# Performance work log

Measured on AMD Instinct MI355X. Metric: run time of the kernel, lower is better.

Reference implementation:

```python
import jax, jax.numpy as jnp
import numpy as np
from jax.scipy.special import logsumexp

_INF = 1e8
_GAMMA_MIN = 1e-4


def _cosine_cost(x, y):
    # 1 - cosine similarity, batched: [B,M,D] x [B,N,D] -> [B,M,N]
    xn = x / jnp.clip(jnp.linalg.norm(x, axis=-1, keepdims=True), 1e-8)
    yn = y / jnp.clip(jnp.linalg.norm(y, axis=-1, keepdims=True), 1e-8)
    return 1.0 - jnp.einsum('bmd,bnd->bmn', xn, yn)


def _soft_dtw_alignment(cost, gv):
    B, M, N = cost.shape
    dt = cost.dtype
    ii = jnp.arange(M)          # full diagonal index range, masked per step

    # ---- forward DP: R[b, i+1, j+1] = C[i,j] + softmin(R[i,j], R[i,j+1], R[i+1,j]) ----
    R0 = jnp.full((B, M + 1, N + 1), _INF, dtype=dt).at[:, 0, 0].set(0.0)

    def fstep(R, d):
        jj = d - ii
        valid = (jj >= 0) & (jj < N)            # (M,)
        jjc = jnp.clip(jj, 0, N - 1)
        ip, jp = ii + 1, jjc + 1
        p = jnp.stack([R[:, ip - 1, jp - 1],
                       R[:, ip - 1, jp],
                       R[:, ip, jp - 1]], axis=-1)          # (B, M, 3)
        soft = -gv * logsumexp(p / -gv, axis=-1)            # soft-min
        new = cost[:, ii, jjc] + soft                       # (B, M)
        cur = R[:, ip, jp]
        R = R.at[:, ip, jp].set(jnp.where(valid[None, :], new, cur))
        return R, None

    R, _ = jax.lax.scan(fstep, R0, jnp.arange(M + N - 1))
    distance = R[:, M, N]

    # ---- backward DP for alignment matrix E ----
    E0 = jnp.zeros((B, M + 2, N + 2), dtype=dt).at[:, M, N].set(1.0)
    Re = jnp.full((B, M + 2, N + 2), -_INF, dtype=dt).at[:, :M + 1, :N + 1].set(R)
    Ce = jnp.zeros((B, M + 2, N + 2), dtype=dt).at[:, 1:M + 1, 1:N + 1].set(cost)

    def bstep(E, d):
        jj = d - ii
        valid = (jj >= 0) & (jj < N)
        jjc = jnp.clip(jj, 0, N - 1)
        ip, jp = ii + 1, jjc + 1
        rc = Re[:, ip, jp]
        wd = jnp.exp(jnp.clip((Re[:, ip + 1, jp + 1] - Ce[:, ip + 1, jp + 1] - rc) / gv, -50, 50))
        wn = jnp.exp(jnp.clip((Re[:, ip + 1, jp] - Ce[:, ip + 1, jp] - rc) / gv, -50, 50))
        wr = jnp.exp(jnp.clip((Re[:, ip, jp + 1] - Ce[:, ip, jp + 1] - rc) / gv, -50, 50))
        new = E[:, ip + 1, jp + 1] * wd + E[:, ip + 1, jp] * wn + E[:, ip, jp + 1] * wr
        cur = E[:, ip, jp]
        E = E.at[:, ip, jp].set(jnp.where(valid[None, :], new, cur))
        return E, None

    E, _ = jax.lax.scan(bstep, E0, jnp.arange(M + N - 3, -1, -1))
    alignment = E[:, 1:M + 1, 1:N + 1]
    return alignment, distance


def setup_inputs() -> dict:
    key = jax.random.key(0)
    k1, k2 = jax.random.split(key)
    B, M, N, D = 8, 256, 256, 512
    x = jax.random.normal(k1, (B, M, D), dtype=jnp.float32)
    y = jax.random.normal(k2, (B, N, D), dtype=jnp.float32)
    gamma = jnp.asarray(1.0, dtype=jnp.float32)   # learned nn.Parameter
    return {"x": x, "y": y, "gamma": gamma}


def reference(x, y, gamma):
    cost = _cosine_cost(x, y)
    gv = jnp.maximum(jnp.abs(gamma), _GAMMA_MIN)   # effective gamma
    alignment, distance = _soft_dtw_alignment(cost, gv)
    return alignment, distance
```

## Files before the change

### kernel.cpp

```cpp
#include <hip/hip_runtime.h>

#define USTR 192

#define EXP2F(x) __builtin_amdgcn_exp2f(x)
#define LOG2F(x) __builtin_amdgcn_logf(x)

__device__ __forceinline__ void ld4(float d[4], const float* p) {
  float4 v = *(const float4*)p;
  d[0] = v.x; d[1] = v.y; d[2] = v.z; d[3] = v.w;
}

__device__ __forceinline__ float dpp_shr1_f(float x) {
  int r = __builtin_amdgcn_update_dpp(0, __float_as_int(x),
                                      0x138 , 0xF, 0xF, true);
  return __int_as_float(r);
}
__device__ __forceinline__ int dpp_shr1_i(int x) {
  return __builtin_amdgcn_update_dpp(0, x, 0x138, 0xF, 0xF, true);
}

__global__ void __launch_bounds__(256) cost_gemm(const float* __restrict__ x,
                                                 const float* __restrict__ y,
                                                 const float* __restrict__ gamma,
                                                 float* __restrict__ mAll) {
  int b = blockIdx.z, mt = blockIdx.y, nt = blockIdx.x;
  int m0 = mt * 32, n0 = nt * 64;
  __shared__ float Xs[2][32][36];
  __shared__ float Ys[2][32][68];
  __shared__ float RxS[32];
  __shared__ float RyS[64];
  int tid = threadIdx.x;
  int row = tid >> 2, cq = tid & 3;
  int tx = tid & 15, ty = tid >> 4;
  const float* xb = x + ((size_t)b * 256 + m0) * 512;
  const float* yb = y + ((size_t)b * 256 + n0) * 512;
  float acc[2][4] = {};
  float sx = 0.f, sy = 0.f;
  float4 xv0, xv1, yv0, yv1;

  auto loadTile = [&](int k0) {
    if (tid < 128) {
      xv0 = *(const float4*)(xb + (size_t)row * 512 + k0 + cq * 4);
      xv1 = *(const float4*)(xb + (size_t)row * 512 + k0 + 16 + cq * 4);
    }
    yv0 = *(const float4*)(yb + (size_t)row * 512 + k0 + cq * 4);
    yv1 = *(const float4*)(yb + (size_t)row * 512 + k0 + 16 + cq * 4);
  };
  auto stageTile = [&](int buf) {
    if (tid < 128) {
      sx += xv0.x*xv0.x + xv0.y*xv0.y + xv0.z*xv0.z + xv0.w*xv0.w
          + xv1.x*xv1.x + xv1.y*xv1.y + xv1.z*xv1.z + xv1.w*xv1.w;
      Xs[buf][cq*4+0][row] = xv0.x; Xs[buf][cq*4+1][row] = xv0.y;
      Xs[buf][cq*4+2][row] = xv0.z; Xs[buf][cq*4+3][row] = xv0.w;
      Xs[buf][16+cq*4+0][row] = xv1.x; Xs[buf][16+cq*4+1][row] = xv1.y;
      Xs[buf][16+cq*4+2][row] = xv1.z; Xs[buf][16+cq*4+3][row] = xv1.w;
    }
    sy += yv0.x*yv0.x + yv0.y*yv0.y + yv0.z*yv0.z + yv0.w*yv0.w
        + yv1.x*yv1.x + yv1.y*yv1.y + yv1.z*yv1.z + yv1.w*yv1.w;
    Ys[buf][cq*4+0][row] = yv0.x; Ys[buf][cq*4+1][row] = yv0.y;
    Ys[buf][cq*4+2][row] = yv0.z; Ys[buf][cq*4+3][row] = yv0.w;
    Ys[buf][16+cq*4+0][row] = yv1.x; Ys[buf][16+cq*4+1][row] = yv1.y;
    Ys[buf][16+cq*4+2][row] = yv1.z; Ys[buf][16+cq*4+3][row] = yv1.w;
  };

  loadTile(0);
  stageTile(0);
  for (int t = 0; t < 16; ++t) {
    __syncthreads();
    if (t < 15) loadTile((t + 1) * 32);
    int cb = t & 1;
#pragma unroll
    for (int kk = 0; kk < 32; ++kk) {
      float2 av = *(const float2*)(&Xs[cb][kk][ty * 2]);
      float4 bv = *(const float4*)(&Ys[cb][kk][tx * 4]);
      acc[0][0] += av.x * bv.x; acc[0][1] += av.x * bv.y;
      acc[0][2] += av.x * bv.z; acc[0][3] += av.x * bv.w;
      acc[1][0] += av.y * bv.x; acc[1][1] += av.y * bv.y;
      acc[1][2] += av.y * bv.z; acc[1][3] += av.y * bv.w;
    }
    if (t < 15) stageTile(cb ^ 1);
  }

  sy += __shfl_xor(sy, 1, 64); sy += __shfl_xor(sy, 2, 64);
  if (tid < 128) { sx += __shfl_xor(sx, 1, 64); sx += __shfl_xor(sx, 2, 64); }
  if (cq == 0) {
    RyS[row] = 1.0f / fmaxf(sqrtf(sy), 1e-8f);
    if (tid < 128) RxS[row] = 1.0f / fmaxf(sqrtf(sx), 1e-8f);
  }
  __syncthreads();

  float gv = fmaxf(fabsf(gamma[0]), 1e-4f);
  float ig2 = 1.4426950408889634f / gv;
  float rx[2], ry[4];
#pragma unroll
  for (int r = 0; r < 2; ++r) rx[r] = RxS[ty * 2 + r];
#pragma unroll
  for (int c = 0; c < 4; ++c) ry[c] = RyS[tx * 4 + c];
  int l = nt * 16 + tx;
  int v = mt * 16 + ty;
  int u = v + l;
  float4 stm[2];
#pragma unroll
  for (int r = 0; r < 2; ++r) {
    float c0 = (1.0f - acc[r][0] * rx[r] * ry[0]) * ig2;
    float c1 = (1.0f - acc[r][1] * rx[r] * ry[1]) * ig2;
    float c2 = (1.0f - acc[r][2] * rx[r] * ry[2]) * ig2;
    float c3 = (1.0f - acc[r][3] * rx[r] * ry[3]) * ig2;
    stm[r] = (float4){EXP2F(-c0), EXP2F(-c1), EXP2F(-c2), EXP2F(-c3)};
  }
  float* mpF = mAll + ((size_t)b * USTR + u) * 512 + l * 8;
  *(float4*)(mpF)     = stm[0];
  *(float4*)(mpF + 4) = stm[1];
}

template<int DIR>
__device__ __forceinline__ void run_chain(const float* __restrict__ mAll,
                                          float* __restrict__ pAll,
                                          float* __restrict__ QepAll,
                                          float gl, int blk, int l,
                                          float* __restrict__ dist_out) {
  int b = blk & 7;
  const float* mb = mAll + (size_t)b * USTR * 512 + (DIR ? (63 - l) * 8 : l * 8);
  float* pb = pAll + (size_t)blk * USTR * 512 + l * 8;
  float* qe = QepAll + ((size_t)blk * 64 + l) * 24;
  float Pp0 = 0.f, Pp1 = 0.f, Pp2 = 0.f, Pp3 = 0.f;
  float bot0 = 0.f, bot1 = 0.f;
  int Q = 0;
  float ucar = (l == 0) ? 1.0f : 0.f;
  float presh0 = 0.f, presh1 = 0.f;
  int adj = 0;
  float A0[8], A1[8], A2[8], A3[8], A4[8], A5[8], A6[8], A7[8];
  float A8[8], A9[8], A10[8], A11[8], A12[8], A13[8], A14[8], A15[8];
  auto loadC = [&](int t, float* buf) {
    int u = t > 190 ? 190 : t;
    int pu = DIR ? 190 - u : u;
    const float* p = mb + (size_t)pu * 512;
    float q0[4], q1[4];
    ld4(q0, p); ld4(q1, p + 4);
    if (DIR) {
      buf[0] = q1[3]; buf[1] = q1[2]; buf[2] = q1[1]; buf[3] = q1[0];
      buf[4] = q0[3]; buf[5] = q0[2]; buf[6] = q0[1]; buf[7] = q0[0];
    } else {
      buf[0] = q0[0]; buf[1] = q0[1]; buf[2] = q0[2]; buf[3] = q0[3];
      buf[4] = q1[0]; buf[5] = q1[1]; buf[6] = q1[2]; buf[7] = q1[3];
    }
  };
  auto body = [&](int t, const float* mm) {
    float s0 = ldexpf(presh0, adj);
    float s1 = ldexpf(presh1, adj);
    float v0 = mm[0] * (Pp0 + s0 + ucar);
    float v1 = mm[1] * (Pp1 + v0 + Pp0);
    float v2 = mm[2] * (Pp2 + v1 + Pp1);
    float v3 = mm[3] * (Pp3 + v2 + Pp2);
    float w0 = mm[4] * (v0 + s1 + s0);
    float w1 = mm[5] * (v1 + w0 + v0);
    float w2 = mm[6] * (v2 + w1 + v1);
    float w3 = mm[7] * (v3 + w2 + v2);
    float* sp = pb + (size_t)t * 512;
    *(float4*)(sp)     = (float4){v0, v1, v2, v3};
    *(float4*)(sp + 4) = (float4){w0, w1, w2, w3};
    Pp0 = w0; Pp1 = w1; Pp2 = w2; Pp3 = w3;
    ucar = s1; bot0 = v3; bot1 = w3;
    if (DIR == 0 && l == 63 && t == 190)
      dist_out[b] = (-(float)Q - LOG2F(w3)) * gl;
    presh0 = dpp_shr1_f(bot0);
    presh1 = dpp_shr1_f(bot1);
  };
  auto renorm = [&](int tEnd) {
    if ((unsigned)(tEnd - l) <= 127u) {
      int e = (int)((__float_as_uint(Pp3) >> 23) & 255u) - 127;
      Pp0 = ldexpf(Pp0, -e); Pp1 = ldexpf(Pp1, -e);
      Pp2 = ldexpf(Pp2, -e); Pp3 = ldexpf(Pp3, -e);
      ucar = ldexpf(ucar, -e);
      bot0 = ldexpf(bot0, -e); bot1 = ldexpf(bot1, -e);
      Q += e;
    }
    presh0 = dpp_shr1_f(bot0);
    presh1 = dpp_shr1_f(bot1);
    adj = dpp_shr1_i(Q) - Q;
  };
  loadC(0, A0);  loadC(1, A1);  loadC(2, A2);  loadC(3, A3);
  loadC(4, A4);  loadC(5, A5);  loadC(6, A6);  loadC(7, A7);
  loadC(8, A8);  loadC(9, A9);  loadC(10, A10); loadC(11, A11);
  loadC(12, A12); loadC(13, A13); loadC(14, A14); loadC(15, A15);
  for (int it = 0; it < 12; ++it) {
    int s = it * 16;
    qe[2 * it] = (float)Q;
    body(s + 0, A0); loadC(s + 16, A0);
    body(s + 1, A1); loadC(s + 17, A1);
    body(s + 2, A2); loadC(s + 18, A2);
    body(s + 3, A3); loadC(s + 19, A3);
    body(s + 4, A4); loadC(s + 20, A4);
    body(s + 5, A5); loadC(s + 21, A5);
    body(s + 6, A6); loadC(s + 22, A6);
    body(s + 7, A7); loadC(s + 23, A7);
    renorm(s + 7);
    qe[2 * it + 1] = (float)Q;
    body(s + 8,  A8);  loadC(s + 24, A8);
    body(s + 9,  A9);  loadC(s + 25, A9);
    body(s + 10, A10); loadC(s + 26, A10);
    body(s + 11, A11); loadC(s + 27, A11);
    body(s + 12, A12); loadC(s + 28, A12);
    body(s + 13, A13); loadC(s + 29, A13);
    body(s + 14, A14); loadC(s + 30, A14);
    body(s + 15, A15); loadC(s + 31, A15);
    renorm(s + 15);
  }
}

__global__ void __launch_bounds__(64, 1) pass_kernel(const float* __restrict__ mAll,
                                                     float* __restrict__ pAll,
                                                     float* __restrict__ QepAll,
                                                     const float* __restrict__ gamma,
                                                     float* __restrict__ dist_out) {
  int blk = blockIdx.x, l = threadIdx.x;
  float gv = fmaxf(fabsf(gamma[0]), 1e-4f);
  float gl = gv * 0.6931471805599453f;
  if (blk < 8) run_chain<0>(mAll, pAll, QepAll, gl, blk, l, dist_out);
  else         run_chain<1>(mAll, pAll, QepAll, gl, blk, l, dist_out);
}

__global__ void __launch_bounds__(256) e_kernel(const float* __restrict__ mAll,
                                                const float* __restrict__ pAll,
                                                const float* __restrict__ QepAll,
                                                float* __restrict__ out) {
  int tid = blockIdx.x * 256 + threadIdx.x;
  int l = tid & 63;
  int r = (tid >> 6) & 255;
  int b = tid >> 14;
  int v = r >> 1, rf = r & 1;
  int uF = v + l;
  int uR = 190 - v - l;
  const float* pF  = pAll + ((size_t)b * USTR + uF) * 512 + l * 8 + rf * 4;
  const float* pRv = pAll + ((size_t)(8 + b) * USTR + uR) * 512 + (63 - l) * 8 + (1 - rf) * 4;
  const float* mF  = mAll + ((size_t)b * USTR + uF) * 512 + l * 8 + rf * 4;
  float P[4], Bv[4], M[4];
  ld4(P, pF); ld4(Bv, pRv); ld4(M, mF);
  float Qf = QepAll[((size_t)b * 64 + l) * 24 + (uF >> 3)];
  float Qb = QepAll[((size_t)(8 + b) * 64 + (63 - l)) * 24 + (uR >> 3)];
  float Zp = pAll[((size_t)b * USTR + 190) * 512 + 511];
  float Zq = QepAll[((size_t)b * 64 + 63) * 24 + 23];
  int e = (int)(Qf + Qb - Zq);
  float inv = 1.0f / Zp;
  float4 o;
  o.x = ldexpf(P[0] * Bv[3] / M[0] * inv, e);
  o.y = ldexpf(P[1] * Bv[2] / M[1] * inv, e);
  o.z = ldexpf(P[2] * Bv[1] / M[2] * inv, e);
  o.w = ldexpf(P[3] * Bv[0] / M[3] * inv, e);
  *(float4*)(out + (size_t)b * 65536 + (size_t)r * 256 + 4 * l) = o;
}

extern "C" void kernel_launch(void* const* d_in, const int* in_sizes, int n_in,
                              void* d_out, int out_size, void* d_ws, size_t ws_size,
                              hipStream_t stream) {
  const float* x = (const float*)d_in[0];
  const float* y = (const float*)d_in[1];
  const float* gamma = (const float*)d_in[2];
  float* out = (float*)d_out;
  float* ws = (float*)d_ws;

  const size_t PMAT_M = (size_t)8 * USTR * 512;
  const size_t PMAT_P = (size_t)16 * USTR * 512;
  float* mAll   = ws + 4096;
  float* pAll   = mAll + PMAT_M;
  float* QepAll = pAll + PMAT_P;

  cost_gemm<<<dim3(4, 8, 8), 256, 0, stream>>>(x, y, gamma, mAll);
  pass_kernel<<<16, 64, 0, stream>>>(mAll, pAll, QepAll, gamma, out + 524288);
  e_kernel<<<512, 256, 0, stream>>>(mAll, pAll, QepAll, out);
}
```

Baseline: 108.0 us.

## Fuse GEMM, DP chain and E-pass into one persistent kernel with grid barriers

```diff
diff --git a/kernel.cpp b/kernel.cpp
--- a/kernel.cpp
+++ b/kernel.cpp
@@ -1,6 +1,7 @@
 #include <hip/hip_runtime.h>
 
 #define USTR 192
+#define NBLK 256
 
 #define EXP2F(x) __builtin_amdgcn_exp2f(x)
 #define LOG2F(x) __builtin_amdgcn_logf(x)
@@ -19,98 +20,23 @@
   return __builtin_amdgcn_update_dpp(0, x, 0x138, 0xF, 0xF, true);
 }
 
-__global__ void __launch_bounds__(256) cost_gemm(const float* __restrict__ x,
-                                                 const float* __restrict__ y,
-                                                 const float* __restrict__ gamma,
-                                                 float* __restrict__ mAll) {
-  int b = blockIdx.z, mt = blockIdx.y, nt = blockIdx.x;
-  int m0 = mt * 32, n0 = nt * 64;
-  __shared__ float Xs[2][32][36];
-  __shared__ float Ys[2][32][68];
-  __shared__ float RxS[32];
-  __shared__ float RyS[64];
-  int tid = threadIdx.x;
-  int row = tid >> 2, cq = tid & 3;
-  int tx = tid & 15, ty = tid >> 4;
-  const float* xb = x + ((size_t)b * 256 + m0) * 512;
-  const float* yb = y + ((size_t)b * 256 + n0) * 512;
-  float acc[2][4] = {};
-  float sx = 0.f, sy = 0.f;
-  float4 xv0, xv1, yv0, yv1;
-
-  auto loadTile = [&](int k0) {
-    if (tid < 128) {
-      xv0 = *(const float4*)(xb + (size_t)row * 512 + k0 + cq * 4);
-      xv1 = *(const float4*)(xb + (size_t)row * 512 + k0 + 16 + cq * 4);
-    }
-    yv0 = *(const float4*)(yb + (size_t)row * 512 + k0 + cq * 4);
-    yv1 = *(const float4*)(yb + (size_t)row * 512 + k0 + 16 + cq * 4);
-  };
-  auto stageTile = [&](int buf) {
-    if (tid < 128) {
-      sx += xv0.x*xv0.x + xv0.y*xv0.y + xv0.z*xv0.z + xv0.w*xv0.w
-          + xv1.x*xv1.x + xv1.y*xv1.y + xv1.z*xv1.z + xv1.w*xv1.w;
-      Xs[buf][cq*4+0][row] = xv0.x; Xs[buf][cq*4+1][row] = xv0.y;
-      Xs[buf][cq*4+2][row] = xv0.z; Xs[buf][cq*4+3][row] = xv0.w;
-      Xs[buf][16+cq*4+0][row] = xv1.x; Xs[buf][16+cq*4+1][row] = xv1.y;
-      Xs[buf][16+cq*4+2][row] = xv1.z; Xs[buf][16+cq*4+3][row] = xv1.w;
-    }
-    sy += yv0.x*yv0.x + yv0.y*yv0.y + yv0.z*yv0.z + yv0.w*yv0.w
-        + yv1.x*yv1.x + yv1.y*yv1.y + yv1.z*yv1.z + yv1.w*yv1.w;
-    Ys[buf][cq*4+0][row] = yv0.x; Ys[buf][cq*4+1][row] = yv0.y;
-    Ys[buf][cq*4+2][row] = yv0.z; Ys[buf][cq*4+3][row] = yv0.w;
-    Ys[buf][16+cq*4+0][row] = yv1.x; Ys[buf][16+cq*4+1][row] = yv1.y;
-    Ys[buf][16+cq*4+2][row] = yv1.z; Ys[buf][16+cq*4+3][row] = yv1.w;
-  };
-
-  loadTile(0);
-  stageTile(0);
-  for (int t = 0; t < 16; ++t) {
-    __syncthreads();
-    if (t < 15) loadTile((t + 1) * 32);
-    int cb = t & 1;
-#pragma unroll
-    for (int kk = 0; kk < 32; ++kk) {
-      float2 av = *(const float2*)(&Xs[cb][kk][ty * 2]);
-      float4 bv = *(const float4*)(&Ys[cb][kk][tx * 4]);
-      acc[0][0] += av.x * bv.x; acc[0][1] += av.x * bv.y;
-      acc[0][2] += av.x * bv.z; acc[0][3] += av.x * bv.w;
-      acc[1][0] += av.y * bv.x; acc[1][1] += av.y * bv.y;
-      acc[1][2] += av.y * bv.z; acc[1][3] += av.y * bv.w;
-    }
-    if (t < 15) stageTile(cb ^ 1);
-  }
-
-  sy += __shfl_xor(sy, 1, 64); sy += __shfl_xor(sy, 2, 64);
-  if (tid < 128) { sx += __shfl_xor(sx, 1, 64); sx += __shfl_xor(sx, 2, 64); }
-  if (cq == 0) {
-    RyS[row] = 1.0f / fmaxf(sqrtf(sy), 1e-8f);
-    if (tid < 128) RxS[row] = 1.0f / fmaxf(sqrtf(sx), 1e-8f);
-  }
+__device__ __forceinline__ void grid_barrier(unsigned* cnt, unsigned* flag) {
   __syncthreads();
-
-  float gv = fmaxf(fabsf(gamma[0]), 1e-4f);
-  float ig2 = 1.4426950408889634f / gv;
-  float rx[2], ry[4];
-#pragma unroll
-  for (int r = 0; r < 2; ++r) rx[r] = RxS[ty * 2 + r];
-#pragma unroll
-  for (int c = 0; c < 4; ++c) ry[c] = RyS[tx * 4 + c];
-  int l = nt * 16 + tx;
-  int v = mt * 16 + ty;
-  int u = v + l;
-  float4 stm[2];
-#pragma unroll
-  for (int r = 0; r < 2; ++r) {
-    float c0 = (1.0f - acc[r][0] * rx[r] * ry[0]) * ig2;
-    float c1 = (1.0f - acc[r][1] * rx[r] * ry[1]) * ig2;
-    float c2 = (1.0f - acc[r][2] * rx[r] * ry[2]) * ig2;
-    float c3 = (1.0f - acc[r][3] * rx[r] * ry[3]) * ig2;
-    stm[r] = (float4){EXP2F(-c0), EXP2F(-c1), EXP2F(-c2), EXP2F(-c3)};
-  }
-  float* mpF = mAll + ((size_t)b * USTR + u) * 512 + l * 8;
-  *(float4*)(mpF)     = stm[0];
-  *(float4*)(mpF + 4) = stm[1];
+  if (threadIdx.x == 0) {
+    unsigned old = __hip_atomic_fetch_add(cnt, 1u, __ATOMIC_ACQ_REL,
+                                          __HIP_MEMORY_SCOPE_AGENT);
+    if (old == NBLK - 1) {
+      __hip_atomic_store(flag, 1u, __ATOMIC_RELEASE, __HIP_MEMORY_SCOPE_AGENT);
+    } else {
+      int guard = 0;
+      while (!__hip_atomic_load(flag, __ATOMIC_ACQUIRE,
+                                __HIP_MEMORY_SCOPE_AGENT)) {
+        __builtin_amdgcn_s_sleep(8);
+        if (++guard > (1 << 22)) break;
+      }
+    }
+  }
+  __syncthreads();
 }
 
 template<int DIR>
@@ -208,46 +134,147 @@
   }
 }
 
-__global__ void __launch_bounds__(64, 1) pass_kernel(const float* __restrict__ mAll,
-                                                     float* __restrict__ pAll,
-                                                     float* __restrict__ QepAll,
-                                                     const float* __restrict__ gamma,
-                                                     float* __restrict__ dist_out) {
-  int blk = blockIdx.x, l = threadIdx.x;
-  float gv = fmaxf(fabsf(gamma[0]), 1e-4f);
-  float gl = gv * 0.6931471805599453f;
-  if (blk < 8) run_chain<0>(mAll, pAll, QepAll, gl, blk, l, dist_out);
-  else         run_chain<1>(mAll, pAll, QepAll, gl, blk, l, dist_out);
-}
-
-__global__ void __launch_bounds__(256) e_kernel(const float* __restrict__ mAll,
-                                                const float* __restrict__ pAll,
-                                                const float* __restrict__ QepAll,
-                                                float* __restrict__ out) {
-  int tid = blockIdx.x * 256 + threadIdx.x;
-  int l = tid & 63;
-  int r = (tid >> 6) & 255;
-  int b = tid >> 14;
-  int v = r >> 1, rf = r & 1;
-  int uF = v + l;
-  int uR = 190 - v - l;
-  const float* pF  = pAll + ((size_t)b * USTR + uF) * 512 + l * 8 + rf * 4;
-  const float* pRv = pAll + ((size_t)(8 + b) * USTR + uR) * 512 + (63 - l) * 8 + (1 - rf) * 4;
-  const float* mF  = mAll + ((size_t)b * USTR + uF) * 512 + l * 8 + rf * 4;
-  float P[4], Bv[4], M[4];
-  ld4(P, pF); ld4(Bv, pRv); ld4(M, mF);
-  float Qf = QepAll[((size_t)b * 64 + l) * 24 + (uF >> 3)];
-  float Qb = QepAll[((size_t)(8 + b) * 64 + (63 - l)) * 24 + (uR >> 3)];
-  float Zp = pAll[((size_t)b * USTR + 190) * 512 + 511];
-  float Zq = QepAll[((size_t)b * 64 + 63) * 24 + 23];
-  int e = (int)(Qf + Qb - Zq);
-  float inv = 1.0f / Zp;
-  float4 o;
-  o.x = ldexpf(P[0] * Bv[3] / M[0] * inv, e);
-  o.y = ldexpf(P[1] * Bv[2] / M[1] * inv, e);
-  o.z = ldexpf(P[2] * Bv[1] / M[2] * inv, e);
-  o.w = ldexpf(P[3] * Bv[0] / M[3] * inv, e);
-  *(float4*)(out + (size_t)b * 65536 + (size_t)r * 256 + 4 * l) = o;
+__global__ void __launch_bounds__(256, 1)
+fused_kernel(const float* __restrict__ x, const float* __restrict__ y,
+             const float* __restrict__ gamma, unsigned* __restrict__ bar,
+             float* __restrict__ mAll, float* __restrict__ pAll,
+             float* __restrict__ QepAll, float* __restrict__ out) {
+
+  {
+    int blk = blockIdx.x;
+    int nt = blk & 3, mt = (blk >> 2) & 7, b = blk >> 5;
+    int m0 = mt * 32, n0 = nt * 64;
+    __shared__ float Xs[2][32][36];
+    __shared__ float Ys[2][32][68];
+    __shared__ float RxS[32];
+    __shared__ float RyS[64];
+    int tid = threadIdx.x;
+    int row = tid >> 2, cq = tid & 3;
+    int tx = tid & 15, ty = tid >> 4;
+    const float* xb = x + ((size_t)b * 256 + m0) * 512;
+    const float* yb = y + ((size_t)b * 256 + n0) * 512;
+    float acc[2][4] = {};
+    float sx = 0.f, sy = 0.f;
+    float4 xv0, xv1, yv0, yv1;
+
+    auto loadTile = [&](int k0) {
+      if (tid < 128) {
+        xv0 = *(const float4*)(xb + (size_t)row * 512 + k0 + cq * 4);
+        xv1 = *(const float4*)(xb + (size_t)row * 512 + k0 + 16 + cq * 4);
+      }
+      yv0 = *(const float4*)(yb + (size_t)row * 512 + k0 + cq * 4);
+      yv1 = *(const float4*)(yb + (size_t)row * 512 + k0 + 16 + cq * 4);
+    };
+    auto stageTile = [&](int buf) {
+      if (tid < 128) {
+        sx += xv0.x*xv0.x + xv0.y*xv0.y + xv0.z*xv0.z + xv0.w*xv0.w
+            + xv1.x*xv1.x + xv1.y*xv1.y + xv1.z*xv1.z + xv1.w*xv1.w;
+        Xs[buf][cq*4+0][row] = xv0.x; Xs[buf][cq*4+1][row] = xv0.y;
+        Xs[buf][cq*4+2][row] = xv0.z; Xs[buf][cq*4+3][row] = xv0.w;
+        Xs[buf][16+cq*4+0][row] = xv1.x; Xs[buf][16+cq*4+1][row] = xv1.y;
+        Xs[buf][16+cq*4+2][row] = xv1.z; Xs[buf][16+cq*4+3][row] = xv1.w;
+      }
+      sy += yv0.x*yv0.x + yv0.y*yv0.y + yv0.z*yv0.z + yv0.w*yv0.w
+          + yv1.x*yv1.x + yv1.y*yv1.y + yv1.z*yv1.z + yv1.w*yv1.w;
+      Ys[buf][cq*4+0][row] = yv0.x; Ys[buf][cq*4+1][row] = yv0.y;
+      Ys[buf][cq*4+2][row] = yv0.z; Ys[buf][cq*4+3][row] = yv0.w;
+      Ys[buf][16+cq*4+0][row] = yv1.x; Ys[buf][16+cq*4+1][row] = yv1.y;
+      Ys[buf][16+cq*4+2][row] = yv1.z; Ys[buf][16+cq*4+3][row] = yv1.w;
+    };
+
+    loadTile(0);
+    stageTile(0);
+    for (int t = 0; t < 16; ++t) {
+      __syncthreads();
+      if (t < 15) loadTile((t + 1) * 32);
+      int cb = t & 1;
+#pragma unroll
+      for (int kk = 0; kk < 32; ++kk) {
+        float2 av = *(const float2*)(&Xs[cb][kk][ty * 2]);
+        float4 bv = *(const float4*)(&Ys[cb][kk][tx * 4]);
+        acc[0][0] += av.x * bv.x; acc[0][1] += av.x * bv.y;
+        acc[0][2] += av.x * bv.z; acc[0][3] += av.x * bv.w;
+        acc[1][0] += av.y * bv.x; acc[1][1] += av.y * bv.y;
+        acc[1][2] += av.y * bv.z; acc[1][3] += av.y * bv.w;
+      }
+      if (t < 15) stageTile(cb ^ 1);
+    }
+
+    sy += __shfl_xor(sy, 1, 64); sy += __shfl_xor(sy, 2, 64);
+    if (tid < 128) { sx += __shfl_xor(sx, 1, 64); sx += __shfl_xor(sx, 2, 64); }
+    if (cq == 0) {
+      RyS[row] = 1.0f / fmaxf(sqrtf(sy), 1e-8f);
+      if (tid < 128) RxS[row] = 1.0f / fmaxf(sqrtf(sx), 1e-8f);
+    }
+    __syncthreads();
+
+    float gv = fmaxf(fabsf(gamma[0]), 1e-4f);
+    float ig2 = 1.4426950408889634f / gv;
+    float rx[2], ry[4];
+#pragma unroll
+    for (int r = 0; r < 2; ++r) rx[r] = RxS[ty * 2 + r];
+#pragma unroll
+    for (int c = 0; c < 4; ++c) ry[c] = RyS[tx * 4 + c];
+    int l = nt * 16 + tx;
+    int v = mt * 16 + ty;
+    int u = v + l;
+    float4 stm[2];
+#pragma unroll
+    for (int r = 0; r < 2; ++r) {
+      float c0 = (1.0f - acc[r][0] * rx[r] * ry[0]) * ig2;
+      float c1 = (1.0f - acc[r][1] * rx[r] * ry[1]) * ig2;
+      float c2 = (1.0f - acc[r][2] * rx[r] * ry[2]) * ig2;
+      float c3 = (1.0f - acc[r][3] * rx[r] * ry[3]) * ig2;
+      stm[r] = (float4){EXP2F(-c0), EXP2F(-c1), EXP2F(-c2), EXP2F(-c3)};
+    }
+    float* mpF = mAll + ((size_t)b * USTR + u) * 512 + l * 8;
+    *(float4*)(mpF)     = stm[0];
+    *(float4*)(mpF + 4) = stm[1];
+  }
+
+  grid_barrier(bar + 0, bar + 1);
+
+  {
+    int blk = blockIdx.x;
+    if (blk < 16 && threadIdx.x < 64) {
+      int l = threadIdx.x;
+      float gv = fmaxf(fabsf(gamma[0]), 1e-4f);
+      float gl = gv * 0.6931471805599453f;
+      float* dist_out = out + 524288;
+      if (blk < 8) run_chain<0>(mAll, pAll, QepAll, gl, blk, l, dist_out);
+      else         run_chain<1>(mAll, pAll, QepAll, gl, blk, l, dist_out);
+    }
+  }
+
+  grid_barrier(bar + 2, bar + 3);
+
+#pragma unroll
+  for (int it = 0; it < 2; ++it) {
+    int tid = (blockIdx.x + (it << 8)) * 256 + threadIdx.x;
+    int l = tid & 63;
+    int r = (tid >> 6) & 255;
+    int b = tid >> 14;
+    int v = r >> 1, rf = r & 1;
+    int uF = v + l;
+    int uR = 190 - v - l;
+    const float* pF  = pAll + ((size_t)b * USTR + uF) * 512 + l * 8 + rf * 4;
+    const float* pRv = pAll + ((size_t)(8 + b) * USTR + uR) * 512 + (63 - l) * 8 + (1 - rf) * 4;
+    const float* mF  = mAll + ((size_t)b * USTR + uF) * 512 + l * 8 + rf * 4;
+    float P[4], Bv[4], M[4];
+    ld4(P, pF); ld4(Bv, pRv); ld4(M, mF);
+    float Qf = QepAll[((size_t)b * 64 + l) * 24 + (uF >> 3)];
+    float Qb = QepAll[((size_t)(8 + b) * 64 + (63 - l)) * 24 + (uR >> 3)];
+    float Zp = pAll[((size_t)b * USTR + 190) * 512 + 511];
+    float Zq = QepAll[((size_t)b * 64 + 63) * 24 + 23];
+    int e = (int)(Qf + Qb - Zq);
+    float inv = 1.0f / Zp;
+    float4 o;
+    o.x = ldexpf(P[0] * Bv[3] / M[0] * inv, e);
+    o.y = ldexpf(P[1] * Bv[2] / M[1] * inv, e);
+    o.z = ldexpf(P[2] * Bv[1] / M[2] * inv, e);
+    o.w = ldexpf(P[3] * Bv[0] / M[3] * inv, e);
+    *(float4*)(out + (size_t)b * 65536 + (size_t)r * 256 + 4 * l) = o;
+  }
 }
 
 extern "C" void kernel_launch(void* const* d_in, const int* in_sizes, int n_in,
@@ -261,11 +288,12 @@
 
   const size_t PMAT_M = (size_t)8 * USTR * 512;
   const size_t PMAT_P = (size_t)16 * USTR * 512;
+  unsigned* bar = (unsigned*)ws;
   float* mAll   = ws + 4096;
   float* pAll   = mAll + PMAT_M;
   float* QepAll = pAll + PMAT_P;
 
-  cost_gemm<<<dim3(4, 8, 8), 256, 0, stream>>>(x, y, gamma, mAll);
-  pass_kernel<<<16, 64, 0, stream>>>(mAll, pAll, QepAll, gamma, out + 524288);
-  e_kernel<<<512, 256, 0, stream>>>(mAll, pAll, QepAll, out);
-}
+  hipMemsetAsync(bar, 0, 4 * sizeof(unsigned), stream);
+  fused_kernel<<<NBLK, 256, 0, stream>>>(x, y, gamma, bar,
+                                         mAll, pAll, QepAll, out);
+}
```

New measurement: 294.4 us. 2.73x slower.
